# Kernel optimization log

Hardware: AMD Instinct MI355X
Metric: run time of the kernel (lower is better)

## Reference

```python
import jax, jax.numpy as jnp
import numpy as np

B, S, N, D_IN, D_OUT = 8, 512, 128, 256, 64
D_HID = D_IN // 2


def setup_inputs() -> dict:
    key = jax.random.key(0)
    ks = jax.random.split(key, 12)
    sc_in = 1.0 / np.sqrt(D_IN)
    sc_hid = 1.0 / np.sqrt(D_HID)
    return {
        "x": jax.random.normal(ks[0], (B, S, N, D_IN), jnp.float32),
        "seq_lengths": jax.random.randint(ks[1], (B,), 0, S),
        # attention1: Linear(D_in, D_hid)
        "W1": jax.random.normal(ks[2], (D_HID, D_IN), jnp.float32) * sc_in,
        "b1": jax.random.normal(ks[3], (D_HID,), jnp.float32) * sc_in,
        # weight_len: (D_hid, 1) xavier param, stored as a vector
        "w_len": jax.random.normal(ks[4], (D_HID,), jnp.float32) * sc_hid,
        # attention: Linear(D_in, D_in)
        "Wa": jax.random.normal(ks[5], (D_IN, D_IN), jnp.float32) * sc_in,
        "ba": jax.random.normal(ks[6], (D_IN,), jnp.float32) * sc_in,
        # embedding: Linear(D_in, D_in)
        "We": jax.random.normal(ks[7], (D_IN, D_IN), jnp.float32) * sc_in,
        "be": jax.random.normal(ks[8], (D_IN,), jnp.float32) * sc_in,
        # fc2: Linear(D_in, D_out)
        "Wf": jax.random.normal(ks[9], (D_OUT, D_IN), jnp.float32) * sc_in,
        "bf": jax.random.normal(ks[10], (D_OUT,), jnp.float32) * sc_in,
    }


def reference(x, seq_lengths, W1, b1, w_len, Wa, ba, We, be, Wf, bf):
    # x: (batch, seq_len, num_nodes, D_in) -- torch code transposes to
    # (num_nodes, seq_len, batch, D_in) then loops nodes; vectorized here.
    b, s, n, d = x.shape
    # final_mask = 11 * (pos < length) - 10  -> 1 where valid, -10 where padded
    pos = jnp.arange(s)
    final_mask = jnp.where(pos[None, :] < seq_lengths[:, None], 1.0, -10.0)  # (b, s)
    # per-node length attention with shared weights
    h = jax.nn.relu(jnp.einsum('bsnd,hd->bsnh', x, W1) + b1)       # (b, s, n, hid)
    scores = jnp.einsum('bsnh,h->bsn', h, w_len)                   # (b, s, n)
    scores = scores * final_mask[:, :, None]
    attn = jax.nn.softmax(scores, axis=1)                           # softmax over seq
    pooled = jnp.einsum('bsnd,bsn->bnd', x, attn)                   # (b, n, d)
    # gated readout (dropout is identity in eval)
    att = jax.nn.sigmoid(pooled @ Wa.T + ba)
    emb = jnp.tanh(pooled @ We.T + be)
    g = (att * emb) @ Wf.T + bf                                     # (b, n, D_out)
    m = jnp.max(g, axis=1)
    return jnp.sum(g, axis=1) / n + m
```

## Files before the change

### kernel.cpp

```cpp
#include <hip/hip_runtime.h>
#include <hip/hip_bf16.h>

#define Bb 8
#define Ss 512
#define Nn 128
#define DIN 256
#define DHID 128
#define DOUT 64

typedef __attribute__((ext_vector_type(8))) __bf16 bf16x8;
typedef __attribute__((ext_vector_type(4))) float f32x4;

__device__ __forceinline__ unsigned short f2bf(float f) {
  unsigned u = __float_as_uint(f);
  u += 0x7fffu + ((u >> 16) & 1u);
  return (unsigned short)(u >> 16);
}
__device__ __forceinline__ float bf2f(unsigned short h) {
  return __uint_as_float(((unsigned)h) << 16);
}

__global__ void prep_w1(const float* __restrict__ W1,
                        unsigned short* __restrict__ w1h,
                        unsigned short* __restrict__ w1l) {
  int i = blockIdx.x * 256 + threadIdx.x;
  float f = W1[i];
  unsigned short h = f2bf(f);
  w1h[i] = h;
  w1l[i] = f2bf(f - bf2f(h));
}

__global__ __launch_bounds__(512) void scores_kernel(
    const float* __restrict__ x, const unsigned short* __restrict__ w1h,
    const unsigned short* __restrict__ w1l, const float* __restrict__ b1,
    const float* __restrict__ wlen, const int* __restrict__ seqlen,
    float* __restrict__ scores) {
  __shared__ unsigned short xs[32 * 520];
  __shared__ float part[8][32];
  const int t = threadIdx.x;
  const int lane = t & 63;
  const int w = t >> 6;
  const int quad = lane >> 4;
  const int l15 = lane & 15;
  const int col = w * 16 + l15;

  bf16x8 bh[8], bl[8];
#pragma unroll
  for (int ks = 0; ks < 8; ++ks) {
    int off = col * 256 + ks * 32 + quad * 8;
    bh[ks] = *(const bf16x8*)(w1h + off);
    bl[ks] = *(const bf16x8*)(w1l + off);
  }
  const float b1c = b1[col];
  const float wlc = wlen[col];

  for (int it = 0; it < 8; ++it) {
    const long tile = (long)blockIdx.x * 8 + it;
    const long m0 = tile * 32;
    const float4* x4 = (const float4*)(x + m0 * DIN);
#pragma unroll
    for (int i = 0; i < 4; ++i) {
      int flat = t + 512 * i;
      int row = flat >> 6, c4 = flat & 63;
      float4 v = x4[flat];
      unsigned short h0 = f2bf(v.x), h1 = f2bf(v.y), h2 = f2bf(v.z), h3 = f2bf(v.w);
      unsigned short g0 = f2bf(v.x - bf2f(h0)), g1 = f2bf(v.y - bf2f(h1));
      unsigned short g2 = f2bf(v.z - bf2f(h2)), g3 = f2bf(v.w - bf2f(h3));
      uint2 ph, pl;
      ph.x = (unsigned)h0 | ((unsigned)h1 << 16);
      ph.y = (unsigned)h2 | ((unsigned)h3 << 16);
      pl.x = (unsigned)g0 | ((unsigned)g1 << 16);
      pl.y = (unsigned)g2 | ((unsigned)g3 << 16);
      *(uint2*)&xs[row * 520 + c4 * 4] = ph;
      *(uint2*)&xs[row * 520 + 256 + c4 * 4] = pl;
    }
    __syncthreads();

#pragma unroll
    for (int mt = 0; mt < 2; ++mt) {
      f32x4 acc = {0.f, 0.f, 0.f, 0.f};
      const int rbase = (mt * 16 + l15) * 520;
#pragma unroll
      for (int ks = 0; ks < 8; ++ks) {
        const int k0 = ks * 32 + quad * 8;
        bf16x8 ah = *(const bf16x8*)&xs[rbase + k0];
        bf16x8 al = *(const bf16x8*)&xs[rbase + 256 + k0];
        acc = __builtin_amdgcn_mfma_f32_16x16x32_bf16(ah, bh[ks], acc, 0, 0, 0);
        acc = __builtin_amdgcn_mfma_f32_16x16x32_bf16(al, bh[ks], acc, 0, 0, 0);
        acc = __builtin_amdgcn_mfma_f32_16x16x32_bf16(ah, bl[ks], acc, 0, 0, 0);
      }
      float p0 = fmaxf(acc[0] + b1c, 0.f) * wlc;
      float p1 = fmaxf(acc[1] + b1c, 0.f) * wlc;
      float p2 = fmaxf(acc[2] + b1c, 0.f) * wlc;
      float p3 = fmaxf(acc[3] + b1c, 0.f) * wlc;
#pragma unroll
      for (int off = 1; off < 16; off <<= 1) {
        p0 += __shfl_xor(p0, off);
        p1 += __shfl_xor(p1, off);
        p2 += __shfl_xor(p2, off);
        p3 += __shfl_xor(p3, off);
      }
      if (l15 < 4) {
        float pv = (l15 == 0) ? p0 : (l15 == 1) ? p1 : (l15 == 2) ? p2 : p3;
        part[w][mt * 16 + quad * 4 + l15] = pv;
      }
    }
    __syncthreads();
    if (t < 32) {
      float v = 0.f;
#pragma unroll
      for (int ww = 0; ww < 8; ++ww) v += part[ww][t];
      long m = m0 + t;
      int b = (int)(m >> 16);
      int s = ((int)m >> 7) & 511;
      float mask = (s < seqlen[b]) ? 1.0f : -10.0f;
      scores[m] = v * mask;
    }
  }
}

__global__ void softmax_kernel(const float* __restrict__ scores,
                               float* __restrict__ attn) {
  const int bi = blockIdx.x;
  const int b = bi >> 7, n = bi & 127;
  const int t = threadIdx.x;
  const float* sp = scores + (long)b * Ss * Nn + n;
  float v0 = sp[(long)t * Nn];
  float v1 = sp[(long)(t + 256) * Nn];
  __shared__ float red[256];
  red[t] = fmaxf(v0, v1);
  __syncthreads();
  for (int o = 128; o > 0; o >>= 1) {
    if (t < o) red[t] = fmaxf(red[t], red[t + o]);
    __syncthreads();
  }
  const float mx = red[0];
  __syncthreads();
  float e0 = expf(v0 - mx), e1 = expf(v1 - mx);
  red[t] = e0 + e1;
  __syncthreads();
  for (int o = 128; o > 0; o >>= 1) {
    if (t < o) red[t] += red[t + o];
    __syncthreads();
  }
  const float inv = 1.0f / red[0];
  float* ap = attn + (long)b * Ss * Nn + n;
  ap[(long)t * Nn] = e0 * inv;
  ap[(long)(t + 256) * Nn] = e1 * inv;
}

__global__ __launch_bounds__(512) void pool_kernel(
    const float* __restrict__ x, const float* __restrict__ attn,
    float* __restrict__ pooled) {
  const int bi = blockIdx.x;
  const int b = bi >> 7, n = bi & 127;
  const int t = threadIdx.x;
  const int sl = t >> 6, d4 = t & 63;
  const float4* xb = (const float4*)x;
  float4 acc = {0.f, 0.f, 0.f, 0.f};
#pragma unroll 4
  for (int s = sl; s < Ss; s += 8) {
    const long row = (long)(b * Ss + s) * Nn + n;
    float a = attn[row];
    float4 v = xb[row * 64 + d4];
    acc.x += a * v.x; acc.y += a * v.y; acc.z += a * v.z; acc.w += a * v.w;
  }
  __shared__ float4 red[8][64];
  red[sl][d4] = acc;
  __syncthreads();
  if (sl == 0) {
    float4 r = red[0][d4];
#pragma unroll
    for (int ww = 1; ww < 8; ++ww) {
      float4 q = red[ww][d4];
      r.x += q.x; r.y += q.y; r.z += q.z; r.w += q.w;
    }
    ((float4*)pooled)[(long)bi * 64 + d4] = r;
  }
}

__global__ void readout_kernel(const float* __restrict__ pooled,
                               const float* __restrict__ Wa, const float* __restrict__ ba,
                               const float* __restrict__ We, const float* __restrict__ be,
                               const float* __restrict__ Wf, const float* __restrict__ bfv,
                               float* __restrict__ g) {
  const int bi = blockIdx.x;
  const int t = threadIdx.x;
  __shared__ __align__(16) float p[256];
  __shared__ __align__(16) float tv[256];
  p[t] = pooled[(long)bi * 256 + t];
  __syncthreads();
  float da = ba[t], de = be[t];
  const float4* pa = (const float4*)p;
  const float4* wa = (const float4*)(Wa + (long)t * 256);
  const float4* we = (const float4*)(We + (long)t * 256);
#pragma unroll 4
  for (int i = 0; i < 64; ++i) {
    float4 pv = pa[i], av = wa[i], ev = we[i];
    da += pv.x * av.x + pv.y * av.y + pv.z * av.z + pv.w * av.w;
    de += pv.x * ev.x + pv.y * ev.y + pv.z * ev.z + pv.w * ev.w;
  }
  float sig = 1.0f / (1.0f + expf(-da));
  float th = tanhf(de);
  tv[t] = sig * th;
  __syncthreads();
  if (t < 64) {
    float go = bfv[t];
    const float4* wf = (const float4*)(Wf + (long)t * 256);
    const float4* tp = (const float4*)tv;
#pragma unroll 4
    for (int i = 0; i < 64; ++i) {
      float4 a = tp[i], q = wf[i];
      go += a.x * q.x + a.y * q.y + a.z * q.z + a.w * q.w;
    }
    g[(long)bi * 64 + t] = go;
  }
}

__global__ void finalize_kernel(const float* __restrict__ g, float* __restrict__ out) {
  const int b = blockIdx.x;
  const int o = threadIdx.x;
  float sum = 0.f, mx = -INFINITY;
  for (int n = 0; n < Nn; ++n) {
    float v = g[((long)b * Nn + n) * DOUT + o];
    sum += v;
    mx = fmaxf(mx, v);
  }
  out[b * DOUT + o] = sum * (1.0f / 128.0f) + mx;
}

extern "C" void kernel_launch(void* const* d_in, const int* in_sizes, int n_in,
                              void* d_out, int out_size, void* d_ws, size_t ws_size,
                              hipStream_t stream) {
  const float* x   = (const float*)d_in[0];
  const int* seql  = (const int*)d_in[1];
  const float* W1  = (const float*)d_in[2];
  const float* b1  = (const float*)d_in[3];
  const float* wl  = (const float*)d_in[4];
  const float* Wa  = (const float*)d_in[5];
  const float* ba  = (const float*)d_in[6];
  const float* We  = (const float*)d_in[7];
  const float* be  = (const float*)d_in[8];
  const float* Wf  = (const float*)d_in[9];
  const float* bfv = (const float*)d_in[10];
  float* out = (float*)d_out;

  char* ws = (char*)d_ws;
  unsigned short* w1h = (unsigned short*)(ws);
  unsigned short* w1l = (unsigned short*)(ws + 65536);
  float* scores = (float*)(ws + 131072);
  float* attn   = (float*)(ws + 131072 + 2097152);
  float* pooled = (float*)(ws + 131072 + 2 * 2097152);
  float* g      = (float*)(ws + 131072 + 2 * 2097152 + 1048576);

  prep_w1<<<128, 256, 0, stream>>>(W1, w1h, w1l);
  scores_kernel<<<2048, 512, 0, stream>>>(x, w1h, w1l, b1, wl, seql, scores);
  softmax_kernel<<<1024, 256, 0, stream>>>(scores, attn);
  pool_kernel<<<1024, 512, 0, stream>>>(x, attn, pooled);
  readout_kernel<<<1024, 256, 0, stream>>>(pooled, Wa, ba, We, be, Wf, bfv, g);
  finalize_kernel<<<8, 64, 0, stream>>>(g, out);
}
```

Baseline: 907.7 us.

## Fuse scores, softmax and pooling into flash-style online-softmax kernel with split-seq combine

```diff
diff --git a/kernel.cpp b/kernel.cpp
--- a/kernel.cpp
+++ b/kernel.cpp
@@ -7,6 +7,8 @@
 #define DIN 256
 #define DHID 128
 #define DOUT 64
+#define TN 16
+#define TS 32
 
 typedef __attribute__((ext_vector_type(8))) __bf16 bf16x8;
 typedef __attribute__((ext_vector_type(4))) float f32x4;
@@ -30,13 +32,14 @@
   w1l[i] = f2bf(f - bf2f(h));
 }
 
-__global__ __launch_bounds__(512) void scores_kernel(
+__global__ __launch_bounds__(512, 4) void flash_kernel(
     const float* __restrict__ x, const unsigned short* __restrict__ w1h,
     const unsigned short* __restrict__ w1l, const float* __restrict__ b1,
     const float* __restrict__ wlen, const int* __restrict__ seqlen,
-    float* __restrict__ scores) {
-  __shared__ unsigned short xs[32 * 520];
-  __shared__ float part[8][32];
+    float* __restrict__ pml, float* __restrict__ pp) {
+  __shared__ unsigned short xs[TN * 520];
+  __shared__ float part[8][TN];
+  __shared__ float alpha_s[TN], ew_s[TN];
   const int t = threadIdx.x;
   const int lane = t & 63;
   const int w = t >> 6;
@@ -44,6 +47,12 @@
   const int l15 = lane & 15;
   const int col = w * 16 + l15;
 
+  const int bi = blockIdx.x;
+  const int b = bi >> 7;
+  const int ng = (bi >> 4) & 7;
+  const int sc = bi & 15;
+  const int slen = seqlen[b];
+
   bf16x8 bh[8], bl[8];
 #pragma unroll
   for (int ks = 0; ks < 8; ++ks) {
@@ -54,13 +63,19 @@
   const float b1c = b1[col];
   const float wlc = wlen[col];
 
-  for (int it = 0; it < 8; ++it) {
-    const long tile = (long)blockIdx.x * 8 + it;
-    const long m0 = tile * 32;
-    const float4* x4 = (const float4*)(x + m0 * DIN);
-#pragma unroll
-    for (int i = 0; i < 4; ++i) {
-      int flat = t + 512 * i;
+  float m_st = -INFINITY, l_st = 0.f;
+  float acc[8];
+#pragma unroll
+  for (int j = 0; j < 8; ++j) acc[j] = 0.f;
+  const int n_l = t >> 5;
+  const int d0 = (t & 31) * 8;
+
+  for (int i = 0; i < TS; ++i) {
+    const int s = sc * TS + i;
+    const float4* x4 = (const float4*)(x + (((long)b * Ss + s) * Nn + ng * TN) * DIN);
+#pragma unroll
+    for (int ii = 0; ii < 2; ++ii) {
+      int flat = t + 512 * ii;
       int row = flat >> 6, c4 = flat & 63;
       float4 v = x4[flat];
       unsigned short h0 = f2bf(v.x), h1 = f2bf(v.y), h2 = f2bf(v.z), h3 = f2bf(v.w);
@@ -76,120 +91,113 @@
     }
     __syncthreads();
 
-#pragma unroll
-    for (int mt = 0; mt < 2; ++mt) {
-      f32x4 acc = {0.f, 0.f, 0.f, 0.f};
-      const int rbase = (mt * 16 + l15) * 520;
-#pragma unroll
-      for (int ks = 0; ks < 8; ++ks) {
-        const int k0 = ks * 32 + quad * 8;
-        bf16x8 ah = *(const bf16x8*)&xs[rbase + k0];
-        bf16x8 al = *(const bf16x8*)&xs[rbase + 256 + k0];
-        acc = __builtin_amdgcn_mfma_f32_16x16x32_bf16(ah, bh[ks], acc, 0, 0, 0);
-        acc = __builtin_amdgcn_mfma_f32_16x16x32_bf16(al, bh[ks], acc, 0, 0, 0);
-        acc = __builtin_amdgcn_mfma_f32_16x16x32_bf16(ah, bl[ks], acc, 0, 0, 0);
+    f32x4 sacc = {0.f, 0.f, 0.f, 0.f};
+#pragma unroll
+    for (int ks = 0; ks < 8; ++ks) {
+      const int k0 = ks * 32 + quad * 8;
+      bf16x8 ah = *(const bf16x8*)&xs[l15 * 520 + k0];
+      bf16x8 al = *(const bf16x8*)&xs[l15 * 520 + 256 + k0];
+      sacc = __builtin_amdgcn_mfma_f32_16x16x32_bf16(ah, bh[ks], sacc, 0, 0, 0);
+      sacc = __builtin_amdgcn_mfma_f32_16x16x32_bf16(al, bh[ks], sacc, 0, 0, 0);
+      sacc = __builtin_amdgcn_mfma_f32_16x16x32_bf16(ah, bl[ks], sacc, 0, 0, 0);
+    }
+    float p0 = fmaxf(sacc[0] + b1c, 0.f) * wlc;
+    float p1 = fmaxf(sacc[1] + b1c, 0.f) * wlc;
+    float p2 = fmaxf(sacc[2] + b1c, 0.f) * wlc;
+    float p3 = fmaxf(sacc[3] + b1c, 0.f) * wlc;
+#pragma unroll
+    for (int off = 1; off < 16; off <<= 1) {
+      p0 += __shfl_xor(p0, off);
+      p1 += __shfl_xor(p1, off);
+      p2 += __shfl_xor(p2, off);
+      p3 += __shfl_xor(p3, off);
+    }
+    if (l15 < 4) {
+      float pv = (l15 == 0) ? p0 : (l15 == 1) ? p1 : (l15 == 2) ? p2 : p3;
+      part[w][quad * 4 + l15] = pv;
+    }
+    __syncthreads();
+
+    if (t < TN) {
+      float raw = 0.f;
+#pragma unroll
+      for (int ww = 0; ww < 8; ++ww) raw += part[ww][t];
+      float mask = (s < slen) ? 1.0f : -10.0f;
+      float scv = raw * mask;
+      float m_new = fmaxf(m_st, scv);
+      float a = expf(m_st - m_new);
+      float e = expf(scv - m_new);
+      l_st = l_st * a + e;
+      m_st = m_new;
+      alpha_s[t] = a;
+      ew_s[t] = e;
+    }
+    __syncthreads();
+
+    {
+      const float a = alpha_s[n_l];
+      const float e = ew_s[n_l];
+      bf16x8 xh = *(const bf16x8*)&xs[n_l * 520 + d0];
+      bf16x8 xl = *(const bf16x8*)&xs[n_l * 520 + 256 + d0];
+#pragma unroll
+      for (int j = 0; j < 8; ++j) {
+        float xv = (float)xh[j] + (float)xl[j];
+        acc[j] = fmaf(acc[j], a, e * xv);
       }
-      float p0 = fmaxf(acc[0] + b1c, 0.f) * wlc;
-      float p1 = fmaxf(acc[1] + b1c, 0.f) * wlc;
-      float p2 = fmaxf(acc[2] + b1c, 0.f) * wlc;
-      float p3 = fmaxf(acc[3] + b1c, 0.f) * wlc;
-#pragma unroll
-      for (int off = 1; off < 16; off <<= 1) {
-        p0 += __shfl_xor(p0, off);
-        p1 += __shfl_xor(p1, off);
-        p2 += __shfl_xor(p2, off);
-        p3 += __shfl_xor(p3, off);
-      }
-      if (l15 < 4) {
-        float pv = (l15 == 0) ? p0 : (l15 == 1) ? p1 : (l15 == 2) ? p2 : p3;
-        part[w][mt * 16 + quad * 4 + l15] = pv;
-      }
-    }
-    __syncthreads();
-    if (t < 32) {
-      float v = 0.f;
-#pragma unroll
-      for (int ww = 0; ww < 8; ++ww) v += part[ww][t];
-      long m = m0 + t;
-      int b = (int)(m >> 16);
-      int s = ((int)m >> 7) & 511;
-      float mask = (s < seqlen[b]) ? 1.0f : -10.0f;
-      scores[m] = v * mask;
-    }
-  }
-}
-
-__global__ void softmax_kernel(const float* __restrict__ scores,
-                               float* __restrict__ attn) {
+    }
+    __syncthreads();
+  }
+
+  {
+    float* dst = pp + ((long)bi * TN + n_l) * 256 + d0;
+    float4 v0 = {acc[0], acc[1], acc[2], acc[3]};
+    float4 v1 = {acc[4], acc[5], acc[6], acc[7]};
+    *(float4*)dst = v0;
+    *(float4*)(dst + 4) = v1;
+  }
+  if (t < TN) {
+    pml[bi * 32 + t] = m_st;
+    pml[bi * 32 + 16 + t] = l_st;
+  }
+}
+
+__global__ __launch_bounds__(256) void combine_readout(
+    const float* __restrict__ pml, const float* __restrict__ pp,
+    const float* __restrict__ Wa, const float* __restrict__ ba,
+    const float* __restrict__ We, const float* __restrict__ be,
+    const float* __restrict__ Wf, const float* __restrict__ bfv,
+    float* __restrict__ g) {
   const int bi = blockIdx.x;
   const int b = bi >> 7, n = bi & 127;
+  const int ng = n >> 4, nl = n & 15;
   const int t = threadIdx.x;
-  const float* sp = scores + (long)b * Ss * Nn + n;
-  float v0 = sp[(long)t * Nn];
-  float v1 = sp[(long)(t + 256) * Nn];
-  __shared__ float red[256];
-  red[t] = fmaxf(v0, v1);
-  __syncthreads();
-  for (int o = 128; o > 0; o >>= 1) {
-    if (t < o) red[t] = fmaxf(red[t], red[t + o]);
-    __syncthreads();
-  }
-  const float mx = red[0];
-  __syncthreads();
-  float e0 = expf(v0 - mx), e1 = expf(v1 - mx);
-  red[t] = e0 + e1;
-  __syncthreads();
-  for (int o = 128; o > 0; o >>= 1) {
-    if (t < o) red[t] += red[t + o];
-    __syncthreads();
-  }
-  const float inv = 1.0f / red[0];
-  float* ap = attn + (long)b * Ss * Nn + n;
-  ap[(long)t * Nn] = e0 * inv;
-  ap[(long)(t + 256) * Nn] = e1 * inv;
-}
-
-__global__ __launch_bounds__(512) void pool_kernel(
-    const float* __restrict__ x, const float* __restrict__ attn,
-    float* __restrict__ pooled) {
-  const int bi = blockIdx.x;
-  const int b = bi >> 7, n = bi & 127;
-  const int t = threadIdx.x;
-  const int sl = t >> 6, d4 = t & 63;
-  const float4* xb = (const float4*)x;
-  float4 acc = {0.f, 0.f, 0.f, 0.f};
-#pragma unroll 4
-  for (int s = sl; s < Ss; s += 8) {
-    const long row = (long)(b * Ss + s) * Nn + n;
-    float a = attn[row];
-    float4 v = xb[row * 64 + d4];
-    acc.x += a * v.x; acc.y += a * v.y; acc.z += a * v.z; acc.w += a * v.w;
-  }
-  __shared__ float4 red[8][64];
-  red[sl][d4] = acc;
-  __syncthreads();
-  if (sl == 0) {
-    float4 r = red[0][d4];
-#pragma unroll
-    for (int ww = 1; ww < 8; ++ww) {
-      float4 q = red[ww][d4];
-      r.x += q.x; r.y += q.y; r.z += q.z; r.w += q.w;
-    }
-    ((float4*)pooled)[(long)bi * 64 + d4] = r;
-  }
-}
-
-__global__ void readout_kernel(const float* __restrict__ pooled,
-                               const float* __restrict__ Wa, const float* __restrict__ ba,
-                               const float* __restrict__ We, const float* __restrict__ be,
-                               const float* __restrict__ Wf, const float* __restrict__ bfv,
-                               float* __restrict__ g) {
-  const int bi = blockIdx.x;
-  const int t = threadIdx.x;
+  __shared__ float coef[16];
   __shared__ __align__(16) float p[256];
   __shared__ __align__(16) float tv[256];
-  p[t] = pooled[(long)bi * 256 + t];
-  __syncthreads();
+
+  if (t < 16) {
+    const int blk = b * 128 + ng * 16 + t;
+    float m = pml[blk * 32 + nl];
+    float l = pml[blk * 32 + 16 + nl];
+    float M = m;
+#pragma unroll
+    for (int off = 1; off < 16; off <<= 1) M = fmaxf(M, __shfl_xor(M, off));
+    float z = l * expf(m - M);
+    float L = z;
+#pragma unroll
+    for (int off = 1; off < 16; off <<= 1) L += __shfl_xor(L, off);
+    coef[t] = expf(m - M) / L;
+  }
+  __syncthreads();
+
+  float accd = 0.f;
+#pragma unroll
+  for (int c = 0; c < 16; ++c) {
+    accd += coef[c] * pp[((long)(b * 128 + ng * 16 + c) * TN + nl) * 256 + t];
+  }
+  p[t] = accd;
+  __syncthreads();
+
   float da = ba[t], de = be[t];
   const float4* pa = (const float4*)p;
   const float4* wa = (const float4*)(Wa + (long)t * 256);
@@ -217,16 +225,29 @@
   }
 }
 
-__global__ void finalize_kernel(const float* __restrict__ g, float* __restrict__ out) {
+__global__ __launch_bounds__(512) void finalize_kernel(const float* __restrict__ g,
+                                                       float* __restrict__ out) {
   const int b = blockIdx.x;
-  const int o = threadIdx.x;
+  const int t = threadIdx.x;
+  const int o = t & 63, ns = t >> 6;
   float sum = 0.f, mx = -INFINITY;
-  for (int n = 0; n < Nn; ++n) {
+  for (int n = ns; n < Nn; n += 8) {
     float v = g[((long)b * Nn + n) * DOUT + o];
     sum += v;
     mx = fmaxf(mx, v);
   }
-  out[b * DOUT + o] = sum * (1.0f / 128.0f) + mx;
+  __shared__ float s1[8][64], s2[8][64];
+  s1[ns][o] = sum;
+  s2[ns][o] = mx;
+  __syncthreads();
+  if (ns == 0) {
+#pragma unroll
+    for (int ww = 1; ww < 8; ++ww) {
+      sum += s1[ww][o];
+      mx = fmaxf(mx, s2[ww][o]);
+    }
+    out[b * 64 + o] = sum * (1.0f / 128.0f) + mx;
+  }
 }
 
 extern "C" void kernel_launch(void* const* d_in, const int* in_sizes, int n_in,
@@ -248,15 +269,12 @@
   char* ws = (char*)d_ws;
   unsigned short* w1h = (unsigned short*)(ws);
   unsigned short* w1l = (unsigned short*)(ws + 65536);
-  float* scores = (float*)(ws + 131072);
-  float* attn   = (float*)(ws + 131072 + 2097152);
-  float* pooled = (float*)(ws + 131072 + 2 * 2097152);
-  float* g      = (float*)(ws + 131072 + 2 * 2097152 + 1048576);
+  float* pml = (float*)(ws + 131072);
+  float* pp  = (float*)(ws + 262144);
+  float* g   = (float*)(ws + 262144 + 16777216);
 
   prep_w1<<<128, 256, 0, stream>>>(W1, w1h, w1l);
-  scores_kernel<<<2048, 512, 0, stream>>>(x, w1h, w1l, b1, wl, seql, scores);
-  softmax_kernel<<<1024, 256, 0, stream>>>(scores, attn);
-  pool_kernel<<<1024, 512, 0, stream>>>(x, attn, pooled);
-  readout_kernel<<<1024, 256, 0, stream>>>(pooled, Wa, ba, We, be, Wf, bfv, g);
-  finalize_kernel<<<8, 64, 0, stream>>>(g, out);
-}
+  flash_kernel<<<1024, 512, 0, stream>>>(x, w1h, w1l, b1, wl, seql, pml, pp);
+  combine_readout<<<1024, 256, 0, stream>>>(pml, pp, Wa, ba, We, be, Wf, bfv, g);
+  finalize_kernel<<<8, 512, 0, stream>>>(g, out);
+}
```

Result: faster. 841.4 us (-7.3%).
